# Optimization experiments

Measured on AMD Instinct MI355X. Metric: run time of the kernel, lower is better.

The kernel has to match this reference:

```python
import jax, jax.numpy as jnp
import numpy as np

DIM = 128
BATCH = 8192
# Static index sets (constants, mirror diag_ind / tril_ind / diag_ind_tril)
TRIL_R, TRIL_C = np.tril_indices(DIM)          # row/col of lower-tri entries, row-major
DIAG_IN_TRIL = np.nonzero(TRIL_R == TRIL_C)[0]  # positions of diagonal entries in flat tril vector
DIAG = np.arange(DIM)
N_TRIL = TRIL_R.size  # dim*(dim+1)/2 = 8256


def setup_inputs() -> dict:
    key = jax.random.key(0)
    x = jax.random.normal(key, (BATCH, N_TRIL), dtype=jnp.float32)
    return {"x": x}


def reference(x):
    # Scatter-fill batched lower-triangular matrix L: [..., DIM, DIM]
    batch_shape = x.shape[:-1]
    L = jnp.zeros(batch_shape + (DIM, DIM), dtype=x.dtype)
    L = L.at[..., TRIL_R, TRIL_C].set(x)
    # Overwrite diagonal with log1p(exp(x_diag) + 1e-12) (softplus-like, as in source)
    diag = jnp.log1p(jnp.exp(x[..., DIAG_IN_TRIL]) + 1e-12)
    L = L.at[..., DIAG, DIAG].set(diag)
    # Diffusion matrix L @ L^T
    return jnp.einsum('...ik,...jk->...ij', L, L)
```

## Files before the change

### kernel.cpp

```cpp
#include <hip/hip_runtime.h>
#include <math.h>


#define DIM       128
#define NTRIL     8256
#define LDS_STRIDE 136
#define ROW_BYTES 272

typedef __bf16 bf16x8 __attribute__((ext_vector_type(8)));
typedef float  f32x16 __attribute__((ext_vector_type(16)));

__global__ __launch_bounds__(256) void tril2diff_kernel(
    const float* __restrict__ x, float* __restrict__ out)
{
    __shared__ alignas(16) __bf16 Lsh[DIM * LDS_STRIDE];

    const int b   = blockIdx.x;
    const int tid = threadIdx.x;

    unsigned int* lz = (unsigned int*)Lsh;
    #pragma unroll
    for (int i = 0; i < 34; ++i)
        lz[tid + i * 256] = 0u;
    __syncthreads();

    const float* xb = x + (size_t)b * NTRIL;
    for (int i = 0; i < 33; ++i) {
        int t = tid + i * 256;
        if (t < NTRIL) {
            float v = xb[t];
            int r = (int)((sqrtf(8.0f * (float)t + 1.0f) - 1.0f) * 0.5f);
            while ((r + 1) * (r + 2) / 2 <= t) ++r;
            while (r * (r + 1) / 2 > t) --r;
            int c = t - r * (r + 1) / 2;
            if (c == r) v = log1pf(expf(v) + 1e-12f);
            Lsh[r * LDS_STRIDE + c] = (__bf16)v;
        }
    }
    __syncthreads();

    const int lane = tid & 63;
    const int wv   = tid >> 6;
    const int i0   = (wv >> 1) * 64;
    const int j0   = (wv & 1) * 64;
    const int cl   = lane & 31;
    const int hh   = lane >> 5;

    f32x16 acc00 = {0}, acc01 = {0}, acc10 = {0}, acc11 = {0};

    const char* lb = (const char*)Lsh;
    #pragma unroll
    for (int ks = 0; ks < 8; ++ks) {
        const int koff = ks * 32 + hh * 16;
        bf16x8 a0 = *(const bf16x8*)(lb + (i0      + cl) * ROW_BYTES + koff);
        bf16x8 a1 = *(const bf16x8*)(lb + (i0 + 32 + cl) * ROW_BYTES + koff);
        bf16x8 b0 = *(const bf16x8*)(lb + (j0      + cl) * ROW_BYTES + koff);
        bf16x8 b1 = *(const bf16x8*)(lb + (j0 + 32 + cl) * ROW_BYTES + koff);
        acc00 = __builtin_amdgcn_mfma_f32_32x32x16_bf16(a0, b0, acc00, 0, 0, 0);
        acc01 = __builtin_amdgcn_mfma_f32_32x32x16_bf16(a0, b1, acc01, 0, 0, 0);
        acc10 = __builtin_amdgcn_mfma_f32_32x32x16_bf16(a1, b0, acc10, 0, 0, 0);
        acc11 = __builtin_amdgcn_mfma_f32_32x32x16_bf16(a1, b1, acc11, 0, 0, 0);
    }

    float* ob = out + (size_t)b * (DIM * DIM);
    #pragma unroll
    for (int reg = 0; reg < 16; ++reg) {
        const int row = (reg & 3) + 8 * (reg >> 2) + 4 * hh;
        ob[(i0      + row) * DIM + j0      + cl] = acc00[reg];
        ob[(i0      + row) * DIM + j0 + 32 + cl] = acc01[reg];
        ob[(i0 + 32 + row) * DIM + j0      + cl] = acc10[reg];
        ob[(i0 + 32 + row) * DIM + j0 + 32 + cl] = acc11[reg];
    }
}

extern "C" void kernel_launch(void* const* d_in, const int* in_sizes, int n_in,
                              void* d_out, int out_size, void* d_ws, size_t ws_size,
                              hipStream_t stream) {
    const float* x = (const float*)d_in[0];
    float* out = (float*)d_out;
    const int batch = in_sizes[0] / NTRIL;
    tril2diff_kernel<<<batch, 256, 0, stream>>>(x, out);
}
```

Baseline: 842.1 us.

## Use constexpr offset table for tril scatter and skip zero-K MFMA blocks

Replaces the per-element sqrt-based row/column recovery with a precomputed constant table of LDS byte offsets. Global loads are now float4 and the LDS zeroing uses 16-byte stores. The diagonal softplus moves to a separate pass over 128 threads. Waves whose 64x64 output tile has zero entries for K>=64 (every block except the lower-right one) skip the upper half of the K loop, exploiting lower-triangular sparsity. The cost is an extra barrier, extra table reads from global memory, and wave divergence in MFMA work across the block.

```diff
diff --git a/kernel.cpp b/kernel.cpp
--- a/kernel.cpp
+++ b/kernel.cpp
@@ -2,13 +2,24 @@
 #include <math.h>
 
 
-#define DIM       128
-#define NTRIL     8256
+#define DIM        128
+#define NTRIL      8256
 #define LDS_STRIDE 136
-#define ROW_BYTES 272
+#define ROW_BYTES  272
 
 typedef __bf16 bf16x8 __attribute__((ext_vector_type(8)));
 typedef float  f32x16 __attribute__((ext_vector_type(16)));
+
+struct RcTab { unsigned short off[NTRIL]; };
+static constexpr RcTab make_tab() {
+    RcTab t{};
+    int idx = 0;
+    for (int r = 0; r < DIM; ++r)
+        for (int c = 0; c <= r; ++c)
+            t.off[idx++] = (unsigned short)((r * LDS_STRIDE + c) * 2);
+    return t;
+}
+__device__ const RcTab TBL = make_tab();
 
 __global__ __launch_bounds__(256) void tril2diff_kernel(
     const float* __restrict__ x, float* __restrict__ out)
@@ -18,24 +29,43 @@
     const int b   = blockIdx.x;
     const int tid = threadIdx.x;
 
-    unsigned int* lz = (unsigned int*)Lsh;
+    uint4* lz4 = (uint4*)Lsh;
     #pragma unroll
-    for (int i = 0; i < 34; ++i)
-        lz[tid + i * 256] = 0u;
+    for (int i = 0; i < 8; ++i)
+        lz4[tid + i * 256] = uint4{0u, 0u, 0u, 0u};
+    if (tid < 128)
+        lz4[2048 + tid] = uint4{0u, 0u, 0u, 0u};
     __syncthreads();
 
     const float* xb = x + (size_t)b * NTRIL;
-    for (int i = 0; i < 33; ++i) {
-        int t = tid + i * 256;
-        if (t < NTRIL) {
-            float v = xb[t];
-            int r = (int)((sqrtf(8.0f * (float)t + 1.0f) - 1.0f) * 0.5f);
-            while ((r + 1) * (r + 2) / 2 <= t) ++r;
-            while (r * (r + 1) / 2 > t) --r;
-            int c = t - r * (r + 1) / 2;
-            if (c == r) v = log1pf(expf(v) + 1e-12f);
-            Lsh[r * LDS_STRIDE + c] = (__bf16)v;
-        }
+    char* lbw = (char*)Lsh;
+    #pragma unroll
+    for (int i = 0; i < 8; ++i) {
+        const int t4 = (tid + i * 256) * 4;
+        const float4  v = *(const float4*)(xb + t4);
+        const ushort4 o = *(const ushort4*)(TBL.off + t4);
+        *(__bf16*)(lbw + o.x) = (__bf16)v.x;
+        *(__bf16*)(lbw + o.y) = (__bf16)v.y;
+        *(__bf16*)(lbw + o.z) = (__bf16)v.z;
+        *(__bf16*)(lbw + o.w) = (__bf16)v.w;
+    }
+    if (tid < 16) {
+        const int t4 = (2048 + tid) * 4;
+        const float4  v = *(const float4*)(xb + t4);
+        const ushort4 o = *(const ushort4*)(TBL.off + t4);
+        *(__bf16*)(lbw + o.x) = (__bf16)v.x;
+        *(__bf16*)(lbw + o.y) = (__bf16)v.y;
+        *(__bf16*)(lbw + o.z) = (__bf16)v.z;
+        *(__bf16*)(lbw + o.w) = (__bf16)v.w;
+    }
+    __syncthreads();
+
+    if (tid < DIM) {
+        const int r = tid;
+        const int t = (r * (r + 1)) / 2 + r;
+        float v = xb[t];
+        v = log1pf(expf(v) + 1e-12f);
+        Lsh[r * LDS_STRIDE + r] = (__bf16)v;
     }
     __syncthreads();
 
@@ -47,20 +77,30 @@
     const int hh   = lane >> 5;
 
     f32x16 acc00 = {0}, acc01 = {0}, acc10 = {0}, acc11 = {0};
+    const char* lb = (const char*)Lsh;
 
-    const char* lb = (const char*)Lsh;
+#define MFMA_STEP(ks)                                                          \
+    {                                                                          \
+        const int koff = (ks) * 32 + hh * 16;                                  \
+        bf16x8 a0 = *(const bf16x8*)(lb + (i0      + cl) * ROW_BYTES + koff);  \
+        bf16x8 a1 = *(const bf16x8*)(lb + (i0 + 32 + cl) * ROW_BYTES + koff);  \
+        bf16x8 b0 = *(const bf16x8*)(lb + (j0      + cl) * ROW_BYTES + koff);  \
+        bf16x8 b1 = *(const bf16x8*)(lb + (j0 + 32 + cl) * ROW_BYTES + koff);  \
+        acc00 = __builtin_amdgcn_mfma_f32_32x32x16_bf16(a0, b0, acc00, 0, 0, 0); \
+        acc01 = __builtin_amdgcn_mfma_f32_32x32x16_bf16(a0, b1, acc01, 0, 0, 0); \
+        acc10 = __builtin_amdgcn_mfma_f32_32x32x16_bf16(a1, b0, acc10, 0, 0, 0); \
+        acc11 = __builtin_amdgcn_mfma_f32_32x32x16_bf16(a1, b1, acc11, 0, 0, 0); \
+    }
+
     #pragma unroll
-    for (int ks = 0; ks < 8; ++ks) {
-        const int koff = ks * 32 + hh * 16;
-        bf16x8 a0 = *(const bf16x8*)(lb + (i0      + cl) * ROW_BYTES + koff);
-        bf16x8 a1 = *(const bf16x8*)(lb + (i0 + 32 + cl) * ROW_BYTES + koff);
-        bf16x8 b0 = *(const bf16x8*)(lb + (j0      + cl) * ROW_BYTES + koff);
-        bf16x8 b1 = *(const bf16x8*)(lb + (j0 + 32 + cl) * ROW_BYTES + koff);
-        acc00 = __builtin_amdgcn_mfma_f32_32x32x16_bf16(a0, b0, acc00, 0, 0, 0);
-        acc01 = __builtin_amdgcn_mfma_f32_32x32x16_bf16(a0, b1, acc01, 0, 0, 0);
-        acc10 = __builtin_amdgcn_mfma_f32_32x32x16_bf16(a1, b0, acc10, 0, 0, 0);
-        acc11 = __builtin_amdgcn_mfma_f32_32x32x16_bf16(a1, b1, acc11, 0, 0, 0);
+    for (int ks = 0; ks < 4; ++ks)
+        MFMA_STEP(ks);
+    if (wv == 3) {
+        #pragma unroll
+        for (int ks = 4; ks < 8; ++ks)
+            MFMA_STEP(ks);
     }
+#undef MFMA_STEP
 
     float* ob = out + (size_t)b * (DIM * DIM);
     #pragma unroll
```

Measured after the change: 687.6 us. -18.4%, faster.
